# Kernel optimization log

Hardware: AMD Instinct MI355X
Metric: run time of the kernel (lower is better)

The kernel has to match this reference:

```python
import jax, jax.numpy as jnp
import numpy as np

HEADS = 16
HEAD_DIM = 128
ROPE_BASE = 10000.0

def _rope_tables(T, D):
    # inv_freq over even indices, freqs = outer(pos, inv_freq), emb = concat([freqs, freqs])
    inv_freq = 1.0 / (ROPE_BASE ** (jnp.arange(0, D, 2, dtype=jnp.float32) / D))
    t = jnp.arange(T, dtype=jnp.float32)
    freqs = t[:, None] * inv_freq[None, :]          # (T, D/2)
    emb = jnp.concatenate([freqs, freqs], axis=-1)  # (T, D)
    return jnp.cos(emb), jnp.sin(emb)

def _rotate_half(x):
    half = x.shape[-1] // 2
    x1, x2 = x[..., :half], x[..., half:]
    return jnp.concatenate([-x2, x1], axis=-1)

def setup_inputs() -> dict:
    key = jax.random.key(0)
    k1, k2, k3 = jax.random.split(key, 3)
    B, T, dim = 2, 2048, 2048
    inner = HEADS * HEAD_DIM
    x = jax.random.normal(k1, (B, T, dim), dtype=jnp.float32)
    W_qkv = jax.random.normal(k2, (3 * inner, dim), dtype=jnp.float32) * 0.02
    W_proj = jax.random.normal(k3, (dim, inner), dtype=jnp.float32) * 0.02
    return {"x": x, "W_qkv": W_qkv, "W_proj": W_proj}

def reference(x, W_qkv, W_proj):
    B, T, dim = x.shape
    H, D = HEADS, HEAD_DIM
    # QKV projection (Linear with weight (out, in): y = x @ W^T)
    qkv = jnp.einsum('btd,ed->bte', x, W_qkv)          # (B, T, 3*H*D)
    q, k, v = jnp.split(qkv, 3, axis=-1)
    def to_heads(t):
        return t.reshape(B, T, H, D).transpose(0, 2, 1, 3)  # (B, H, T, D)
    q, k, v = to_heads(q), to_heads(k), to_heads(v)
    # RoPE, offset = 0 (uncached path)
    cos, sin = _rope_tables(T, D)                      # (T, D)
    cos = cos[None, None]
    sin = sin[None, None]
    q = q * cos + _rotate_half(q) * sin
    k = k * cos + _rotate_half(k) * sin
    # causal SDPA
    scale = 1.0 / jnp.sqrt(jnp.float32(D))
    scores = jnp.einsum('bhqd,bhkd->bhqk', q, k) * scale
    causal = jnp.tril(jnp.ones((T, T), dtype=bool))
    scores = jnp.where(causal[None, None], scores, jnp.finfo(scores.dtype).min)
    attn = jax.nn.softmax(scores, axis=-1)
    out = jnp.einsum('bhqk,bhkd->bhqd', attn, v)       # (B, H, T, D)
    out = out.transpose(0, 2, 1, 3).reshape(B, T, H * D)
    return jnp.einsum('bti,oi->bto', out, W_proj)      # (B, T, dim)
```

## Files before the change

kernel.cpp:

```cpp
#include <hip/hip_runtime.h>
#include <hip/hip_bf16.h>
#include <stdint.h>

typedef __attribute__((ext_vector_type(8))) short short8;
typedef __attribute__((ext_vector_type(4))) short short4v;
typedef __attribute__((ext_vector_type(4))) float f32x4;

#define HEADS 16
#define HDIM  128
#define BB    2
#define TT    2048
#define DMODEL 2048
#define INNER 2048
#define E3    6144
#define NTOK  (BB*TT)

__device__ inline void store1(__hip_bfloat16* p, float v) { *p = __float2bfloat16(v); }
__device__ inline void store1(float* p, float v)          { *p = v; }

__device__ inline short bfbits(float v) {
  __hip_bfloat16 h = __float2bfloat16(v);
  return *(short*)&h;
}

__device__ inline void gl_lds16(const __hip_bfloat16* g, __hip_bfloat16* l) {
  __builtin_amdgcn_global_load_lds(
      (const __attribute__((address_space(1))) void*)g,
      (__attribute__((address_space(3))) void*)l, 16, 0, 0);
}

__device__ inline void cvt8(const float* in, __hip_bfloat16* out, int i) {
  float4 a = *(const float4*)(in + i);
  float4 b = *(const float4*)(in + i + 4);
  short8 r;
  r[0]=bfbits(a.x); r[1]=bfbits(a.y); r[2]=bfbits(a.z); r[3]=bfbits(a.w);
  r[4]=bfbits(b.x); r[5]=bfbits(b.y); r[6]=bfbits(b.z); r[7]=bfbits(b.w);
  *(short8*)(out + i) = r;
}

#define NBX   (NTOK*DMODEL/2048)
#define NBW   (E3*DMODEL/2048)
#define NBT   (TT*64/256)
__global__ __launch_bounds__(256)
void prep(const float* __restrict__ x, const float* __restrict__ Wqkv,
          __hip_bfloat16* __restrict__ xb, __hip_bfloat16* __restrict__ Wqkvb,
          float2* __restrict__ tab)
{
  const int tid = threadIdx.x;
  int blk = blockIdx.x;
  if (blk < NBX) {
    cvt8(x, xb, (blk*256 + tid)*8);
  } else if (blk < NBX + NBW) {
    cvt8(Wqkv, Wqkvb, ((blk-NBX)*256 + tid)*8);
  } else {
    int idx = (blk - NBX - NBW)*256 + tid;
    int t  = idx >> 6;
    int d2 = idx & 63;
    float inv = powf(10000.f, -(float)d2 * (1.f/64.f));
    float ang = (float)t * inv;
    tab[idx] = make_float2(cosf(ang), sinf(ang));
  }
}

__global__ __launch_bounds__(256)
void cvt_bf16(const float* __restrict__ in, __hip_bfloat16* __restrict__ out, int n)
{
  int i = (blockIdx.x * 256 + threadIdx.x) * 8;
  if (i >= n) return;
  cvt8(in, out, i);
}

template<typename TC>
__global__ __launch_bounds__(256, 2)
void gemm_lds(const __hip_bfloat16* __restrict__ A,
              const __hip_bfloat16* __restrict__ B,
              TC* __restrict__ C,
              int M, int N, int K)
{
  __shared__ __hip_bfloat16 sA[128*32];
  __shared__ __hip_bfloat16 sB[128*32];
  const int tid  = threadIdx.x;
  const int lane = tid & 63;
  const int wv   = tid >> 6;
  const int lm   = lane & 15;
  const int quad = lane >> 4;
  const int wm   = (wv >> 1) * 64;
  const int wn   = (wv & 1) * 64;
  const int bm   = blockIdx.y * 128;
  const int bn   = blockIdx.x * 128;

  f32x4 acc[4][4];
  #pragma unroll
  for (int i=0;i<4;i++)
    #pragma unroll
    for (int j=0;j<4;j++) acc[i][j] = (f32x4){0.f,0.f,0.f,0.f};

  const int srow = wv*32 + (lane >> 2);
  const int scol = (lane & 3) * 8;
  const __hip_bfloat16* gA0 = A + (size_t)(bm + srow)*K + scol;
  const __hip_bfloat16* gA1 = gA0 + (size_t)16*K;
  const __hip_bfloat16* gB0 = B + (size_t)(bn + srow)*K + scol;
  const __hip_bfloat16* gB1 = gB0 + (size_t)16*K;
  __hip_bfloat16* lA0 = sA + wv*1024;
  __hip_bfloat16* lA1 = lA0 + 512;
  __hip_bfloat16* lB0 = sB + wv*1024;
  __hip_bfloat16* lB1 = lB0 + 512;

  for (int k0 = 0; k0 < K; k0 += 32) {
    __syncthreads();
    gl_lds16(gA0, lA0);
    gl_lds16(gA1, lA1);
    gl_lds16(gB0, lB0);
    gl_lds16(gB1, lB1);
    gA0 += 32; gA1 += 32; gB0 += 32; gB1 += 32;
    __syncthreads();
    short8 af[4], bf[4];
    #pragma unroll
    for (int t=0;t<4;t++)
      af[t] = *(const short8*)(sA + (wm + t*16 + lm)*32 + quad*8);
    #pragma unroll
    for (int t=0;t<4;t++)
      bf[t] = *(const short8*)(sB + (wn + t*16 + lm)*32 + quad*8);
    #pragma unroll
    for (int i=0;i<4;i++)
      #pragma unroll
      for (int j=0;j<4;j++)
        acc[i][j] = __builtin_amdgcn_mfma_f32_16x16x32_bf16(af[i], bf[j], acc[i][j], 0,0,0);
  }

  const int row0 = bm + wm + quad*4;
  const int col0 = bn + wn + lm;
  #pragma unroll
  for (int i=0;i<4;i++)
    #pragma unroll
    for (int j=0;j<4;j++)
      #pragma unroll
      for (int r=0;r<4;r++)
        store1(C + (size_t)(row0 + i*16 + r)*N + col0 + j*16, acc[i][j][r]);
}

__global__ __launch_bounds__(512, 2)
void gemm_qkv3(const __hip_bfloat16* __restrict__ A,
               const __hip_bfloat16* __restrict__ B,
               const float2* __restrict__ tab,
               __hip_bfloat16* __restrict__ Qh,
               __hip_bfloat16* __restrict__ Kh,
               __hip_bfloat16* __restrict__ Vt)
{
  __shared__ __align__(128) __hip_bfloat16 smem[49152];
  const int tid  = threadIdx.x;
  const int lane = tid & 63;
  const int w    = tid >> 6;
  const int lm   = lane & 15;
  const int quad = lane >> 4;
  const int wm   = w >> 2;
  const int wn   = w & 3;

  const int flat  = blockIdx.x;
  const int wgid  = (flat & 7) * 96 + (flat >> 3);
  const int tileN = wgid >> 5;
  const int tileM = wgid & 31;
  const int bm    = tileM << 7;
  const int bn    = tileN << 8;
  const int type  = bn >> 11;

  const int r0 = tid >> 3;
  const int kc = (tid & 7) ^ (r0 & 7);
  const size_t gA0 = ((size_t)(bm      + r0) << 11) + kc*8;
  const size_t gA1 = ((size_t)(bm + 64 + r0) << 11) + kc*8;
  size_t gB[2][2];
  #pragma unroll
  for (int h = 0; h < 2; ++h)
    #pragma unroll
    for (int j = 0; j < 2; ++j) {
      int prow;
      if (type < 2)
        prow = h*128 + j*32 + ((r0 >> 5) << 6) + (((r0 >> 4) & 1) << 4) + (r0 & 15);
      else
        prow = h*128 + j*64 + r0;
      gB[h][j] = ((size_t)(bn + prow) << 11) + kc*8;
    }
  const int ldsW = w * 512;

#define STAGE_A(ktt, bb_) do { \
    __hip_bfloat16* _l = smem + (bb_)*24576 + ldsW; \
    gl_lds16(A + gA0 + (size_t)(ktt)*64, _l); \
    gl_lds16(A + gA1 + (size_t)(ktt)*64, _l + 4096); \
  } while (0)
#define STAGE_B(h, ktt, bb_) do { \
    __hip_bfloat16* _l = smem + (bb_)*24576 + 8192 + (h)*8192 + ldsW; \
    gl_lds16(B + gB[h][0] + (size_t)(ktt)*64, _l); \
    gl_lds16(B + gB[h][1] + (size_t)(ktt)*64, _l + 4096); \
  } while (0)

  const int xk0 = ((quad      ^ (lm & 7)) << 3);
  const int xk1 = (((quad|4)  ^ (lm & 7)) << 3);
  const int aRow = wm*4096 + lm*64;
  const int bRow = 8192 + (wn>>1)*8192 + (wn&1)*4096 + lm*64;

  f32x4 acc[4][4];
  #pragma unroll
  for (int i=0;i<4;i++)
    #pragma unroll
    for (int j=0;j<4;j++) acc[i][j] = (f32x4){0.f,0.f,0.f,0.f};

  STAGE_A(0, 0);
  STAGE_B(0, 0, 0);
  STAGE_B(1, 0, 0);
  STAGE_A(1, 1);
  asm volatile("s_waitcnt vmcnt(2)" ::: "memory");
  __builtin_amdgcn_s_barrier();

  #pragma unroll 2
  for (int kt = 0; kt < 32; ++kt) {
    const int cb   = kt & 1;
    const int nb   = cb ^ 1;
    const int cOff = cb * 24576;

    short8 a0[4], b0[4], a1[4], b1[4];
    #pragma unroll
    for (int f = 0; f < 4; ++f) {
      a0[f] = *(const short8*)(smem + cOff + aRow + f*1024 + xk0);
      b0[f] = *(const short8*)(smem + cOff + bRow + f*1024 + xk0);
    }
    #pragma unroll
    for (int f = 0; f < 4; ++f) {
      a1[f] = *(const short8*)(smem + cOff + aRow + f*1024 + xk1);
      b1[f] = *(const short8*)(smem + cOff + bRow + f*1024 + xk1);
    }
    if (kt + 1 < 32) STAGE_B(0, kt+1, nb);
    __builtin_amdgcn_s_barrier();
    __builtin_amdgcn_s_setprio(1);
    #pragma unroll
    for (int i = 0; i < 4; ++i)
      #pragma unroll
      for (int j = 0; j < 4; ++j)
        acc[i][j] = __builtin_amdgcn_mfma_f32_16x16x32_bf16(a0[i], b0[j], acc[i][j], 0,0,0);
    __builtin_amdgcn_s_setprio(0);
    __builtin_amdgcn_s_barrier();

    if (kt + 1 < 32) STAGE_B(1, kt+1, nb);
    if (kt + 2 < 32) STAGE_A(kt+2, cb);
    __builtin_amdgcn_s_barrier();
    __builtin_amdgcn_s_setprio(1);
    #pragma unroll
    for (int i = 0; i < 4; ++i)
      #pragma unroll
      for (int j = 0; j < 4; ++j)
        acc[i][j] = __builtin_amdgcn_mfma_f32_16x16x32_bf16(a1[i], b1[j], acc[i][j], 0,0,0);
    __builtin_amdgcn_s_setprio(0);
    if (kt < 30) asm volatile("s_waitcnt vmcnt(2)" ::: "memory");
    else         asm volatile("s_waitcnt vmcnt(0)" ::: "memory");
    __builtin_amdgcn_s_barrier();
  }
#undef STAGE_A
#undef STAGE_B

  const float SCQ = 0.08838834764831845f * 1.4426950408889634f;
  const int tok0 = bm + wm*64;
  if (type < 2) {
    __hip_bfloat16* const dst = (type == 0) ? Qh : Kh;
    const float mul = (type == 0) ? SCQ : 1.0f;
    const int head = ((bn & 2047) >> 7) + (wn >> 1);
    const int d2b  = (wn & 1)*32 + lm;
    #pragma unroll
    for (int i = 0; i < 4; ++i) {
      #pragma unroll
      for (int r = 0; r < 4; ++r) {
        const int t  = tok0 + i*16 + quad*4 + r;
        const int b  = t >> 11;
        const int tl = t & (TT-1);
        const float2* tp = tab + (size_t)tl*64;
        __hip_bfloat16* const o = dst + ((size_t)(b*HEADS + head)*TT + tl)*HDIM;
        #pragma unroll
        for (int j = 0; j < 2; ++j) {
          const int d2 = d2b + j*16;
          const float2 cs = tp[d2];
          const float v1 = acc[i][j  ][r];
          const float v2 = acc[i][j+2][r];
          o[d2]      = __float2bfloat16((v1*cs.x - v2*cs.y) * mul);
          o[d2 + 64] = __float2bfloat16((v2*cs.x + v1*cs.y) * mul);
        }
      }
    }
  } else {
    const int fcb = (bn & 2047) + wn*64 + lm;
    #pragma unroll
    for (int i = 0; i < 4; ++i) {
      const int t0 = tok0 + i*16 + quad*4;
      const int b  = t0 >> 11;
      const int tl = t0 & (TT-1);
      #pragma unroll
      for (int j = 0; j < 4; ++j) {
        const int c    = fcb + j*16;
        const int head = c >> 7;
        const int d    = c & 127;
        short4v o;
        #pragma unroll
        for (int r = 0; r < 4; ++r) o[r] = bfbits(acc[i][j][r]);
        *(short4v*)(Vt + ((size_t)(b*HEADS + head)*HDIM + d)*TT + tl) = o;
      }
    }
  }
}

__global__ __launch_bounds__(256, 3)
void flash_attn4(const __hip_bfloat16* __restrict__ Qh,
                 const __hip_bfloat16* __restrict__ Kh,
                 const __hip_bfloat16* __restrict__ Vt,
                 __hip_bfloat16* __restrict__ Out)
{
  const int tid  = threadIdx.x;
  const int lane = tid & 63;
  const int wv   = tid >> 6;
  const int lm   = lane & 15;
  const int quad = lane >> 4;
  const int jA   = blockIdx.x;
  const int bh   = blockIdx.y;
  const int b    = bh >> 4;
  const int h    = bh & 15;

  __shared__ __hip_bfloat16 sK[64*136];
  __shared__ __hip_bfloat16 sV[128*72];
  __shared__ __hip_bfloat16 sP[4][16*72];

  const float FML2 = 8.0f * 1.4426950408889634f;

  const int rk0 = tid >> 4;
  const int ck  = (tid & 15) * 8;
  const int dv0 = tid >> 3;
  const int cv  = (tid & 7) * 8;
  const __hip_bfloat16* KpBase = Kh + (size_t)bh*TT*HDIM + (size_t)rk0*HDIM + ck;
  const __hip_bfloat16* VpBase = Vt + (size_t)bh*HDIM*TT + (size_t)dv0*TT + cv;

  #pragma unroll
  for (int pass = 0; pass < 2; ++pass) {
    const int q0 = (pass == 0 ? jA : 31 - jA) * 64;

    short8 aq[4];
    {
      const __hip_bfloat16* qp = Qh + ((size_t)bh*TT + q0 + wv*16 + lm)*HDIM + quad*8;
      #pragma unroll
      for (int kd=0;kd<4;kd++) aq[kd] = *(const short8*)(qp + kd*32);
    }

    float l_p = 0.f;
    f32x4 acc_o[8];
    #pragma unroll
    for (int i=0;i<8;i++) acc_o[i] = (f32x4){0.f,0.f,0.f,0.f};

    const __hip_bfloat16* Kp = KpBase;
    const __hip_bfloat16* Vp = VpBase;
    short8 pk[4], pv[4];
    #pragma unroll
    for (int it=0;it<4;++it) {
      pk[it] = *(const short8*)(Kp + (size_t)it*16*HDIM);
      pv[it] = *(const short8*)(Vp + (size_t)it*32*TT);
    }
    Kp += (size_t)64*HDIM; Vp += 64;

    for (int kv0 = 0; kv0 <= q0; kv0 += 64) {
      __syncthreads();
      #pragma unroll
      for (int it=0;it<4;++it) {
        *(short8*)(&sK[(it*16 + rk0)*136 + ck]) = pk[it];
        *(short8*)(&sV[(it*32 + dv0)*72 + cv])  = pv[it];
      }
      if (kv0 + 64 <= q0) {
        #pragma unroll
        for (int it=0;it<4;++it) {
          pk[it] = *(const short8*)(Kp + (size_t)it*16*HDIM);
          pv[it] = *(const short8*)(Vp + (size_t)it*32*TT);
        }
        Kp += (size_t)64*HDIM; Vp += 64;
      }
      __syncthreads();

      f32x4 accs[4];
      #pragma unroll
      for (int nt=0;nt<4;nt++) accs[nt] = (f32x4){0.f,0.f,0.f,0.f};
      __builtin_amdgcn_s_setprio(1);
      #pragma unroll
      for (int kd=0;kd<4;kd++)
        #pragma unroll
        for (int nt=0;nt<4;nt++) {
          short8 bk = *(const short8*)(&sK[(nt*16 + lm)*136 + kd*32 + quad*8]);
          accs[nt] = __builtin_amdgcn_mfma_f32_16x16x32_bf16(bk, aq[kd], accs[nt], 0,0,0);
        }
      __builtin_amdgcn_s_setprio(0);

      const int qcol = q0 + wv*16 + lm;
      const bool diag = (kv0 == q0);
      #pragma unroll
      for (int nt=0;nt<4;nt++) {
        short4v w;
        #pragma unroll
        for (int r=0;r<4;r++) {
          float p = exp2f(accs[nt][r] - FML2);
          if (diag && (kv0 + nt*16 + quad*4 + r > qcol)) p = 0.f;
          l_p += p;
          w[r] = bfbits(p);
        }
        *(short4v*)(&sP[wv][lm*72 + nt*16 + quad*4]) = w;
      }

      short8 ap0 = *(const short8*)(&sP[wv][lm*72 + quad*8]);
      short8 ap1 = *(const short8*)(&sP[wv][lm*72 + 32 + quad*8]);
      __builtin_amdgcn_s_setprio(1);
      #pragma unroll
      for (int nt2=0;nt2<8;nt2++) {
        short8 bvv = *(const short8*)(&sV[(nt2*16 + lm)*72 + quad*8]);
        acc_o[nt2] = __builtin_amdgcn_mfma_f32_16x16x32_bf16(ap0, bvv, acc_o[nt2], 0,0,0);
      }
      #pragma unroll
      for (int nt2=0;nt2<8;nt2++) {
        short8 bvv = *(const short8*)(&sV[(nt2*16 + lm)*72 + 32 + quad*8]);
        acc_o[nt2] = __builtin_amdgcn_mfma_f32_16x16x32_bf16(ap1, bvv, acc_o[nt2], 0,0,0);
      }
      __builtin_amdgcn_s_setprio(0);
    }

    l_p += __shfl_xor(l_p, 16);
    l_p += __shfl_xor(l_p, 32);
    const float linv = 1.f / l_p;
    float inv[4];
    #pragma unroll
    for (int r=0;r<4;r++) inv[r] = __shfl(linv, quad*4 + r);

    #pragma unroll
    for (int nt2=0;nt2<8;nt2++)
      #pragma unroll
      for (int r=0;r<4;r++) {
        int t = q0 + wv*16 + quad*4 + r;
        Out[((size_t)b*TT + t)*INNER + (size_t)h*HDIM + nt2*16 + lm] =
          __float2bfloat16(acc_o[nt2][r] * inv[r]);
      }
  }
}

extern "C" void kernel_launch(void* const* d_in, const int* in_sizes, int n_in,
                              void* d_out, int out_size, void* d_ws, size_t ws_size,
                              hipStream_t stream)
{
  (void)in_sizes; (void)n_in; (void)out_size; (void)ws_size;
  const float* x     = (const float*)d_in[0];
  const float* Wqkv  = (const float*)d_in[1];
  const float* Wproj = (const float*)d_in[2];
  float* out = (float*)d_out;

  char* ws = (char*)d_ws;
  __hip_bfloat16* xb       = (__hip_bfloat16*)ws;
  __hip_bfloat16* attn_out = xb;
  char* p1 = ws + (size_t)NTOK*DMODEL*2;
  __hip_bfloat16* Wqkvb  = (__hip_bfloat16*)p1;
  __hip_bfloat16* Wprojb = (__hip_bfloat16*)p1;
  char* p2 = p1 + (size_t)E3*DMODEL*2;
  float2* ropeTab = (float2*)p2;
  char* p3 = p2 + (size_t)DMODEL*INNER*2;
  const size_t hsz = (size_t)BB*HEADS*TT*HDIM*2;
  __hip_bfloat16* Qh = (__hip_bfloat16*)p3;
  __hip_bfloat16* Kh = (__hip_bfloat16*)(p3 + hsz);
  __hip_bfloat16* Vt = (__hip_bfloat16*)(p3 + 2*hsz);

  prep<<<dim3(NBX + NBW + NBT), dim3(256), 0, stream>>>(x, Wqkv, xb, Wqkvb, ropeTab);

  gemm_qkv3<<<dim3(768), dim3(512), 0, stream>>>(xb, Wqkvb, ropeTab, Qh, Kh, Vt);

  cvt_bf16<<<dim3(DMODEL*INNER/2048), dim3(256), 0, stream>>>(Wproj, Wprojb, DMODEL*INNER);

  flash_attn4<<<dim3(TT/128, BB*HEADS), dim3(256), 0, stream>>>(Qh, Kh, Vt, attn_out);

  gemm_lds<float>
    <<<dim3(INNER/128, NTOK/128), dim3(256), 0, stream>>>(attn_out, Wprojb, out, NTOK, INNER, DMODEL);
}
```

Before: 375.1 us.

## Replace output projection GEMM with double-buffered 512-thread pipelined kernel

Swaps the simple single-buffered 128x128 projection GEMM for a 128x256-tile, 8-wave kernel. It uses double-buffered LDS with a 64-wide K step, XOR-swizzled LDS layout, and interleaved async global-to-LDS loads between MFMA phases with priority hints. A grouped block-index mapping improves L2 reuse. The aim is to hide load latency and cut LDS bank conflicts and barrier stalls, at the cost of more LDS per block and hard-coded dimensions.

```diff
diff --git a/kernel.cpp b/kernel.cpp
--- a/kernel.cpp
+++ b/kernel.cpp
@@ -14,9 +14,6 @@
 #define INNER 2048
 #define E3    6144
 #define NTOK  (BB*TT)
-
-__device__ inline void store1(__hip_bfloat16* p, float v) { *p = __float2bfloat16(v); }
-__device__ inline void store1(float* p, float v)          { *p = v; }
 
 __device__ inline short bfbits(float v) {
   __hip_bfloat16 h = __float2bfloat16(v);
@@ -70,75 +67,6 @@
   cvt8(in, out, i);
 }
 
-template<typename TC>
-__global__ __launch_bounds__(256, 2)
-void gemm_lds(const __hip_bfloat16* __restrict__ A,
-              const __hip_bfloat16* __restrict__ B,
-              TC* __restrict__ C,
-              int M, int N, int K)
-{
-  __shared__ __hip_bfloat16 sA[128*32];
-  __shared__ __hip_bfloat16 sB[128*32];
-  const int tid  = threadIdx.x;
-  const int lane = tid & 63;
-  const int wv   = tid >> 6;
-  const int lm   = lane & 15;
-  const int quad = lane >> 4;
-  const int wm   = (wv >> 1) * 64;
-  const int wn   = (wv & 1) * 64;
-  const int bm   = blockIdx.y * 128;
-  const int bn   = blockIdx.x * 128;
-
-  f32x4 acc[4][4];
-  #pragma unroll
-  for (int i=0;i<4;i++)
-    #pragma unroll
-    for (int j=0;j<4;j++) acc[i][j] = (f32x4){0.f,0.f,0.f,0.f};
-
-  const int srow = wv*32 + (lane >> 2);
-  const int scol = (lane & 3) * 8;
-  const __hip_bfloat16* gA0 = A + (size_t)(bm + srow)*K + scol;
-  const __hip_bfloat16* gA1 = gA0 + (size_t)16*K;
-  const __hip_bfloat16* gB0 = B + (size_t)(bn + srow)*K + scol;
-  const __hip_bfloat16* gB1 = gB0 + (size_t)16*K;
-  __hip_bfloat16* lA0 = sA + wv*1024;
-  __hip_bfloat16* lA1 = lA0 + 512;
-  __hip_bfloat16* lB0 = sB + wv*1024;
-  __hip_bfloat16* lB1 = lB0 + 512;
-
-  for (int k0 = 0; k0 < K; k0 += 32) {
-    __syncthreads();
-    gl_lds16(gA0, lA0);
-    gl_lds16(gA1, lA1);
-    gl_lds16(gB0, lB0);
-    gl_lds16(gB1, lB1);
-    gA0 += 32; gA1 += 32; gB0 += 32; gB1 += 32;
-    __syncthreads();
-    short8 af[4], bf[4];
-    #pragma unroll
-    for (int t=0;t<4;t++)
-      af[t] = *(const short8*)(sA + (wm + t*16 + lm)*32 + quad*8);
-    #pragma unroll
-    for (int t=0;t<4;t++)
-      bf[t] = *(const short8*)(sB + (wn + t*16 + lm)*32 + quad*8);
-    #pragma unroll
-    for (int i=0;i<4;i++)
-      #pragma unroll
-      for (int j=0;j<4;j++)
-        acc[i][j] = __builtin_amdgcn_mfma_f32_16x16x32_bf16(af[i], bf[j], acc[i][j], 0,0,0);
-  }
-
-  const int row0 = bm + wm + quad*4;
-  const int col0 = bn + wn + lm;
-  #pragma unroll
-  for (int i=0;i<4;i++)
-    #pragma unroll
-    for (int j=0;j<4;j++)
-      #pragma unroll
-      for (int r=0;r<4;r++)
-        store1(C + (size_t)(row0 + i*16 + r)*N + col0 + j*16, acc[i][j][r]);
-}
-
 __global__ __launch_bounds__(512, 2)
 void gemm_qkv3(const __hip_bfloat16* __restrict__ A,
                const __hip_bfloat16* __restrict__ B,
@@ -304,6 +232,124 @@
   }
 }
 
+__global__ __launch_bounds__(512, 2)
+void gemm_proj(const __hip_bfloat16* __restrict__ A,
+               const __hip_bfloat16* __restrict__ B,
+               float* __restrict__ C)
+{
+  __shared__ __align__(128) __hip_bfloat16 smem[49152];
+  const int tid  = threadIdx.x;
+  const int lane = tid & 63;
+  const int w    = tid >> 6;
+  const int lm   = lane & 15;
+  const int quad = lane >> 4;
+  const int wm   = w >> 2;
+  const int wn   = w & 3;
+
+  const int flat  = blockIdx.x;
+  const int wgid  = (flat & 7) * 32 + (flat >> 3);
+  const int tileN = wgid >> 5;
+  const int tileM = wgid & 31;
+  const int bm    = tileM << 7;
+  const int bn    = tileN << 8;
+
+  const int r0 = tid >> 3;
+  const int kc = (tid & 7) ^ (r0 & 7);
+  const size_t gA0 = ((size_t)(bm      + r0) << 11) + kc*8;
+  const size_t gA1 = ((size_t)(bm + 64 + r0) << 11) + kc*8;
+  size_t gB[2][2];
+  #pragma unroll
+  for (int h = 0; h < 2; ++h)
+    #pragma unroll
+    for (int j = 0; j < 2; ++j)
+      gB[h][j] = ((size_t)(bn + h*128 + j*64 + r0) << 11) + kc*8;
+  const int ldsW = w * 512;
+
+#define STAGE_A(ktt, bb_) do { \
+    __hip_bfloat16* _l = smem + (bb_)*24576 + ldsW; \
+    gl_lds16(A + gA0 + (size_t)(ktt)*64, _l); \
+    gl_lds16(A + gA1 + (size_t)(ktt)*64, _l + 4096); \
+  } while (0)
+#define STAGE_B(h, ktt, bb_) do { \
+    __hip_bfloat16* _l = smem + (bb_)*24576 + 8192 + (h)*8192 + ldsW; \
+    gl_lds16(B + gB[h][0] + (size_t)(ktt)*64, _l); \
+    gl_lds16(B + gB[h][1] + (size_t)(ktt)*64, _l + 4096); \
+  } while (0)
+
+  const int xk0 = ((quad      ^ (lm & 7)) << 3);
+  const int xk1 = (((quad|4)  ^ (lm & 7)) << 3);
+  const int aRow = wm*4096 + lm*64;
+  const int bRow = 8192 + (wn>>1)*8192 + (wn&1)*4096 + lm*64;
+
+  f32x4 acc[4][4];
+  #pragma unroll
+  for (int i=0;i<4;i++)
+    #pragma unroll
+    for (int j=0;j<4;j++) acc[i][j] = (f32x4){0.f,0.f,0.f,0.f};
+
+  STAGE_A(0, 0);
+  STAGE_B(0, 0, 0);
+  STAGE_B(1, 0, 0);
+  STAGE_A(1, 1);
+  asm volatile("s_waitcnt vmcnt(2)" ::: "memory");
+  __builtin_amdgcn_s_barrier();
+
+  #pragma unroll 2
+  for (int kt = 0; kt < 32; ++kt) {
+    const int cb   = kt & 1;
+    const int nb   = cb ^ 1;
+    const int cOff = cb * 24576;
+
+    short8 a0[4], b0[4], a1[4], b1[4];
+    #pragma unroll
+    for (int f = 0; f < 4; ++f) {
+      a0[f] = *(const short8*)(smem + cOff + aRow + f*1024 + xk0);
+      b0[f] = *(const short8*)(smem + cOff + bRow + f*1024 + xk0);
+    }
+    #pragma unroll
+    for (int f = 0; f < 4; ++f) {
+      a1[f] = *(const short8*)(smem + cOff + aRow + f*1024 + xk1);
+      b1[f] = *(const short8*)(smem + cOff + bRow + f*1024 + xk1);
+    }
+    if (kt + 1 < 32) STAGE_B(0, kt+1, nb);
+    __builtin_amdgcn_s_barrier();
+    __builtin_amdgcn_s_setprio(1);
+    #pragma unroll
+    for (int i = 0; i < 4; ++i)
+      #pragma unroll
+      for (int j = 0; j < 4; ++j)
+        acc[i][j] = __builtin_amdgcn_mfma_f32_16x16x32_bf16(a0[i], b0[j], acc[i][j], 0,0,0);
+    __builtin_amdgcn_s_setprio(0);
+    __builtin_amdgcn_s_barrier();
+
+    if (kt + 1 < 32) STAGE_B(1, kt+1, nb);
+    if (kt + 2 < 32) STAGE_A(kt+2, cb);
+    __builtin_amdgcn_s_barrier();
+    __builtin_amdgcn_s_setprio(1);
+    #pragma unroll
+    for (int i = 0; i < 4; ++i)
+      #pragma unroll
+      for (int j = 0; j < 4; ++j)
+        acc[i][j] = __builtin_amdgcn_mfma_f32_16x16x32_bf16(a1[i], b1[j], acc[i][j], 0,0,0);
+    __builtin_amdgcn_s_setprio(0);
+    if (kt < 30) asm volatile("s_waitcnt vmcnt(2)" ::: "memory");
+    else         asm volatile("s_waitcnt vmcnt(0)" ::: "memory");
+    __builtin_amdgcn_s_barrier();
+  }
+#undef STAGE_A
+#undef STAGE_B
+
+  const int tok0 = bm + wm*64;
+  const int coln = bn + wn*64 + lm;
+  #pragma unroll
+  for (int i = 0; i < 4; ++i)
+    #pragma unroll
+    for (int j = 0; j < 4; ++j)
+      #pragma unroll
+      for (int r = 0; r < 4; ++r)
+        C[(size_t)(tok0 + i*16 + quad*4 + r)*INNER + coln + j*16] = acc[i][j][r];
+}
+
 __global__ __launch_bounds__(256, 3)
 void flash_attn4(const __hip_bfloat16* __restrict__ Qh,
                  const __hip_bfloat16* __restrict__ Kh,
@@ -470,6 +516,5 @@
 
   flash_attn4<<<dim3(TT/128, BB*HEADS), dim3(256), 0, stream>>>(Qh, Kh, Vt, attn_out);
 
-  gemm_lds<float>
-    <<<dim3(INNER/128, NTOK/128), dim3(256), 0, stream>>>(attn_out, Wprojb, out, NTOK, INNER, DMODEL);
-}
+  gemm_proj<<<dim3(256), dim3(512), 0, stream>>>(attn_out, Wprojb, out);
+}
```

Result: faster. 365.3 us (-2.6%).
